# Optimization experiments

Measured on AMD Instinct MI355X. Metric: run time of the kernel, lower is better.

The kernel has to match this reference:

```python
import jax, jax.numpy as jnp
import numpy as np


def _w16_to_4():
    # Constant 4x16 projection from 16 gate logits to {1, A, B, A*B} coefficients
    W = np.zeros((4, 16), np.float32)
    W[0, 8:16] = 1
    W[1, [2, 3, 6, 7]] = 1
    W[1, [8, 9, 12, 13]] = -1
    W[2, [4, 5, 6, 7]] = 1
    W[2, [8, 9, 10, 11]] = -1
    W[3, 1] = 1
    W[3, 6] = -2
    W[3, [2, 4, 7, 14]] = -1
    W[3, [1, 8, 11, 13]] = 1
    W[3, 9] = 2
    return jnp.asarray(W)

W16_TO_4 = _w16_to_4()
G_SPARSITY = 1.0


def _layer(x, idx, w):
    # x: [B, in], idx: [2G] gather indices, w: [16, G]
    B = x.shape[0]
    xg = x[:, idx].reshape(B, -1, 2)          # [B, G, 2]
    A = xg[..., 0]
    Bv = xg[..., 1]
    s = jax.nn.softmax(w * G_SPARSITY, axis=0)  # [16, G]
    w4 = W16_TO_4 @ s                           # [4, G]
    return w4[0] + w4[1] * A + w4[2] * Bv + w4[3] * (A * Bv)  # [B, G]


def setup_inputs() -> dict:
    key = jax.random.key(0)
    B, IN, G, L = 2048, 1024, 16384, 6
    ks = jax.random.split(key, 2 * L + 3)
    inp = {"x": jax.random.uniform(ks[0], (B, IN), dtype=jnp.float32)}
    for l in range(L):
        hi = IN if l == 0 else G
        inp[f"idx{l}"] = jax.random.randint(ks[1 + l], (2 * G,), 0, hi, dtype=jnp.int32)
        inp[f"w{l}"] = jax.random.normal(ks[1 + L + l], (16, G), dtype=jnp.float32)
    inp["lin_w"] = jax.random.normal(ks[-2], (G, 1), dtype=jnp.float32) * 0.01
    inp["lin_b"] = jnp.zeros((1,), dtype=jnp.float32)
    return inp


def reference(x, w0, w1, w2, w3, w4, w5, lin_w, lin_b,
              idx0, idx1, idx2, idx3, idx4, idx5):
    ws = [w0, w1, w2, w3, w4, w5]
    idxs = [idx0, idx1, idx2, idx3, idx4, idx5]
    for w, idx in zip(ws, idxs):
        x = _layer(x, idx, w)
    return x @ lin_w + lin_b  # [B, 1]
```

## Files before the change

### kernel.cpp

```cpp
#include <hip/hip_runtime.h>
#include <hip/hip_fp16.h>

#define G_DIM 16384
#define N_BATCH 2048
#define IN_DIM 1024
#define NLAYER 6
#define THREADS 1024
#define GPT 16
#define CHUNK 4
#define NCHUNK (GPT / CHUNK)
#define ROWS 4

struct Ptrs {
    const int*   idx[NLAYER];
    const float* w[NLAYER];
};

__device__ __forceinline__ unsigned f2h(float a, float b) {
    __half2 h = __floats2half2_rn(a, b);
    return *reinterpret_cast<unsigned*>(&h);
}

__device__ __forceinline__ float mix_hlh(unsigned a, unsigned b, unsigned c) {
    float d;
    asm("v_fma_mix_f32 %0, %1, %2, %3 op_sel:[1,0,1] op_sel_hi:[1,1,1]"
        : "=v"(d) : "v"(a), "v"(b), "v"(c));
    return d;
}
__device__ __forceinline__ float mix_hhh(unsigned a, unsigned b, unsigned c) {
    float d;
    asm("v_fma_mix_f32 %0, %1, %2, %3 op_sel:[1,1,1] op_sel_hi:[1,1,1]"
        : "=v"(d) : "v"(a), "v"(b), "v"(c));
    return d;
}
__device__ __forceinline__ float mix_lll(unsigned a, unsigned b, unsigned c) {
    float d;
    asm("v_fma_mix_f32 %0, %1, %2, %3 op_sel:[0,0,0] op_sel_hi:[1,1,1]"
        : "=v"(d) : "v"(a), "v"(b), "v"(c));
    return d;
}
__device__ __forceinline__ float mix_lhl(unsigned a, unsigned b, unsigned c) {
    float d;
    asm("v_fma_mix_f32 %0, %1, %2, %3 op_sel:[0,1,0] op_sel_hi:[1,1,1]"
        : "=v"(d) : "v"(a), "v"(b), "v"(c));
    return d;
}
__device__ __forceinline__ float mix_alo(float u, unsigned A, float v) {
    float d;
    asm("v_fma_mix_f32 %0, %1, %2, %3 op_sel:[0,0,0] op_sel_hi:[0,1,0]"
        : "=v"(d) : "v"(u), "v"(A), "v"(v));
    return d;
}
__device__ __forceinline__ float mix_ahi(float u, unsigned A, float v) {
    float d;
    asm("v_fma_mix_f32 %0, %1, %2, %3 op_sel:[0,1,0] op_sel_hi:[0,1,0]"
        : "=v"(d) : "v"(u), "v"(A), "v"(v));
    return d;
}
__device__ __forceinline__ unsigned mix_pack(float u0, float v0, float u1, float v1,
                                             unsigned A) {
    unsigned t;
    asm("v_fma_mixlo_f16 %0, %1, %2, %3 op_sel:[0,0,0] op_sel_hi:[0,1,0]"
        : "=v"(t) : "v"(u0), "v"(A), "v"(v0));
    asm("v_fma_mixhi_f16 %0, %1, %2, %3 op_sel:[0,1,0] op_sel_hi:[0,1,0]"
        : "+v"(t) : "v"(u1), "v"(A), "v"(v1));
    return t;
}

__device__ __forceinline__ float4 softmax_coef(const float* __restrict__ w, int g) {
    float v[16];
    float m = -1e30f;
#pragma unroll
    for (int k = 0; k < 16; ++k) { v[k] = w[k * G_DIM + g]; m = fmaxf(m, v[k]); }
    float s = 0.f;
#pragma unroll
    for (int k = 0; k < 16; ++k) { v[k] = expf(v[k] - m); s += v[k]; }
    const float inv = 1.f / s;
    float4 c;
    c.x = (v[8]+v[9]+v[10]+v[11]+v[12]+v[13]+v[14]+v[15]) * inv;
    c.y = (v[2]+v[3]+v[6]+v[7] - v[8]-v[9]-v[12]-v[13]) * inv;
    c.z = (v[4]+v[5]+v[6]+v[7] - v[8]-v[9]-v[10]-v[11]) * inv;
    c.w = (v[1]-v[2]-v[4]-2.f*v[6]-v[7]+v[8]+2.f*v[9]+v[11]+v[13]-v[14]) * inv;
    return c;
}

__global__ __launch_bounds__(256) void pack_kernel(Ptrs P, uint2* __restrict__ hcf,
                                                   unsigned* __restrict__ sidx) {
    const int g = blockIdx.x * blockDim.x + threadIdx.x;
    const int l = blockIdx.y;
    const float4 c = softmax_coef(P.w[l], g);
    hcf[(size_t)l * G_DIM + g] = make_uint2(f2h(c.x, c.y), f2h(c.z, c.w));
    const int2 p = ((const int2*)P.idx[l])[g];
    sidx[(size_t)l * G_DIM + g] = (unsigned)p.x | ((unsigned)p.y << 16);
}

__global__ __launch_bounds__(THREADS) void fused_ws_kernel(
    const float* __restrict__ x,
    const uint2* __restrict__ hcf,
    const unsigned* __restrict__ sidx,
    const float* __restrict__ lin_w,
    const float* __restrict__ lin_b,
    float* __restrict__ out)
{
    __shared__ uint2 buf[G_DIM];
    __shared__ float red[ROWS][THREADS / 64];

    const int tid  = threadIdx.x;
    const int row0 = blockIdx.x * ROWS;

#pragma unroll
    for (int i = tid; i < IN_DIM; i += THREADS) {
        const float r0 = x[(size_t)(row0 + 0) * IN_DIM + i];
        const float r1 = x[(size_t)(row0 + 1) * IN_DIM + i];
        const float r2 = x[(size_t)(row0 + 2) * IN_DIM + i];
        const float r3 = x[(size_t)(row0 + 3) * IN_DIM + i];
        buf[i] = make_uint2(f2h(r0, r1), f2h(r2, r3));
    }

    unsigned pk[CHUNK];
    uint2    cc[CHUNK];
#pragma unroll
    for (int j = 0; j < CHUNK; ++j) {
        pk[j] = sidx[tid + j * THREADS];
        cc[j] = hcf[tid + j * THREADS];
    }

    __syncthreads();

    float a0 = 0.f, a1 = 0.f, a2 = 0.f, a3 = 0.f;

#pragma unroll
    for (int l = 0; l < NLAYER; ++l) {
        const uint2*    __restrict__ cl = hcf  + (size_t)l * G_DIM;
        const unsigned* __restrict__ sl = sidx + (size_t)l * G_DIM;
        uint2 o[GPT];

#pragma unroll
        for (int ch = 0; ch < NCHUNK; ++ch) {
            unsigned pkn[CHUNK];
            uint2    ccn[CHUNK];
            if (ch + 1 < NCHUNK) {
#pragma unroll
                for (int j = 0; j < CHUNK; ++j) {
                    pkn[j] = sl[tid + ((ch + 1) * CHUNK + j) * THREADS];
                    ccn[j] = cl[tid + ((ch + 1) * CHUNK + j) * THREADS];
                }
            } else if (l + 1 < NLAYER) {
                const unsigned* __restrict__ sn = sidx + (size_t)(l + 1) * G_DIM;
                const uint2*    __restrict__ cn = hcf  + (size_t)(l + 1) * G_DIM;
#pragma unroll
                for (int j = 0; j < CHUNK; ++j) {
                    pkn[j] = sn[tid + j * THREADS];
                    ccn[j] = cn[tid + j * THREADS];
                }
            }

            float lw[CHUNK];
            if (l == NLAYER - 1) {
#pragma unroll
                for (int j = 0; j < CHUNK; ++j)
                    lw[j] = lin_w[tid + (ch * CHUNK + j) * THREADS];
            }

#pragma unroll
            for (int j = 0; j < CHUNK; ++j) {
                const uint2 Au = buf[pk[j] & 0xFFFFu];
                const uint2 Bu = buf[pk[j] >> 16];
                const unsigned c01 = cc[j].x;
                const unsigned c23 = cc[j].y;
                const float u0 = mix_hlh(c23, Bu.x, c01);
                const float u1 = mix_hhh(c23, Bu.x, c01);
                const float v0 = mix_lll(c23, Bu.x, c01);
                const float v1 = mix_lhl(c23, Bu.x, c01);
                const float u2 = mix_hlh(c23, Bu.y, c01);
                const float u3 = mix_hhh(c23, Bu.y, c01);
                const float v2 = mix_lll(c23, Bu.y, c01);
                const float v3 = mix_lhl(c23, Bu.y, c01);
                if (l < NLAYER - 1) {
                    const unsigned t01 = mix_pack(u0, v0, u1, v1, Au.x);
                    const unsigned t23 = mix_pack(u2, v2, u3, v3, Au.y);
                    o[ch * CHUNK + j] = make_uint2(t01, t23);
                } else {
                    const float o0 = mix_alo(u0, Au.x, v0);
                    const float o1 = mix_ahi(u1, Au.x, v1);
                    const float o2 = mix_alo(u2, Au.y, v2);
                    const float o3 = mix_ahi(u3, Au.y, v3);
                    a0 = fmaf(o0, lw[j], a0);
                    a1 = fmaf(o1, lw[j], a1);
                    a2 = fmaf(o2, lw[j], a2);
                    a3 = fmaf(o3, lw[j], a3);
                }
            }

            if (ch + 1 < NCHUNK || l + 1 < NLAYER) {
#pragma unroll
                for (int j = 0; j < CHUNK; ++j) { pk[j] = pkn[j]; cc[j] = ccn[j]; }
            }
        }

        if (l < NLAYER - 1) {
            __syncthreads();
#pragma unroll
            for (int i = 0; i < GPT; ++i) buf[tid + i * THREADS] = o[i];
            __syncthreads();
        }
    }

#pragma unroll
    for (int off = 32; off > 0; off >>= 1) {
        a0 += __shfl_down(a0, off);
        a1 += __shfl_down(a1, off);
        a2 += __shfl_down(a2, off);
        a3 += __shfl_down(a3, off);
    }
    const int lane = tid & 63, wid = tid >> 6;
    if (lane == 0) { red[0][wid] = a0; red[1][wid] = a1; red[2][wid] = a2; red[3][wid] = a3; }
    __syncthreads();
    if (tid < ROWS) {
        float s = 0.f;
#pragma unroll
        for (int k = 0; k < THREADS / 64; ++k) s += red[tid][k];
        out[row0 + tid] = s + lin_b[0];
    }
}

__global__ __launch_bounds__(THREADS, 1) void fused_fallback_kernel(
    const float* __restrict__ x, Ptrs P,
    const float* __restrict__ lin_w, const float* __restrict__ lin_b,
    float* __restrict__ out)
{
    __shared__ float2 buf[G_DIM];
    __shared__ float red0[THREADS / 64];
    __shared__ float red1[THREADS / 64];
    const int tid  = threadIdx.x;
    const int row0 = blockIdx.x * 2;
    for (int i = tid; i < IN_DIM; i += THREADS)
        buf[i] = make_float2(x[(size_t)row0 * IN_DIM + i],
                             x[(size_t)(row0 + 1) * IN_DIM + i]);
    __syncthreads();
    float2 o[GPT];
    for (int l = 0; l < NLAYER; ++l) {
        const int2* __restrict__ idxl = (const int2*)P.idx[l];
#pragma unroll
        for (int i = 0; i < GPT; ++i) {
            const int g = tid + i * THREADS;
            const int2 p = idxl[g];
            const float4 c = softmax_coef(P.w[l], g);
            const float2 Ap = buf[p.x];
            const float2 Bp = buf[p.y];
            o[i].x = fmaf(fmaf(c.w, Bp.x, c.y), Ap.x, fmaf(c.z, Bp.x, c.x));
            o[i].y = fmaf(fmaf(c.w, Bp.y, c.y), Ap.y, fmaf(c.z, Bp.y, c.x));
        }
        __syncthreads();
#pragma unroll
        for (int i = 0; i < GPT; ++i) buf[tid + i * THREADS] = o[i];
        __syncthreads();
    }
    float a0 = 0.f, a1 = 0.f;
#pragma unroll
    for (int i = 0; i < GPT; ++i) {
        const int g = tid + i * THREADS;
        const float lw = lin_w[g];
        const float2 bv = buf[g];
        a0 = fmaf(bv.x, lw, a0);
        a1 = fmaf(bv.y, lw, a1);
    }
#pragma unroll
    for (int off = 32; off > 0; off >>= 1) {
        a0 += __shfl_down(a0, off);
        a1 += __shfl_down(a1, off);
    }
    const int lane = tid & 63, wid = tid >> 6;
    if (lane == 0) { red0[wid] = a0; red1[wid] = a1; }
    __syncthreads();
    if (tid == 0) {
        float s0 = 0.f, s1 = 0.f;
#pragma unroll
        for (int k = 0; k < THREADS / 64; ++k) { s0 += red0[k]; s1 += red1[k]; }
        const float lb = lin_b[0];
        out[row0]     = s0 + lb;
        out[row0 + 1] = s1 + lb;
    }
}

extern "C" void kernel_launch(void* const* d_in, const int* in_sizes, int n_in,
                              void* d_out, int out_size, void* d_ws, size_t ws_size,
                              hipStream_t stream) {
    const float* x = (const float*)d_in[0];
    Ptrs P;
    for (int l = 0; l < NLAYER; ++l) {
        P.idx[l] = (const int*)d_in[1 + 2 * l];
        P.w[l]   = (const float*)d_in[2 + 2 * l];
    }
    const float* lin_w = (const float*)d_in[13];
    const float* lin_b = (const float*)d_in[14];
    float* out = (float*)d_out;

    const size_t hcf_bytes  = (size_t)NLAYER * G_DIM * sizeof(uint2);
    const size_t sidx_bytes = (size_t)NLAYER * G_DIM * sizeof(unsigned);
    if (ws_size >= hcf_bytes + sidx_bytes) {
        uint2*    hcf  = (uint2*)d_ws;
        unsigned* sidx = (unsigned*)((char*)d_ws + hcf_bytes);
        dim3 cgrid(G_DIM / 256, NLAYER);
        pack_kernel<<<cgrid, 256, 0, stream>>>(P, hcf, sidx);
        fused_ws_kernel<<<N_BATCH / ROWS, THREADS, 0, stream>>>(
            x, hcf, sidx, lin_w, lin_b, out);
    } else {
        fused_fallback_kernel<<<N_BATCH / 2, THREADS, 0, stream>>>(
            x, P, lin_w, lin_b, out);
    }
}
```

Before: 56.36 us.

## Assign gate pairs per thread with vectorized loads and software-pipelined LDS gathers

Each thread now handles adjacent gate pairs, so index, coefficient, lin_w and LDS output traffic use 64/128-bit vector loads and stores (uint2/uint4/float2) instead of scalar ones. The gather from shared memory is software-pipelined: the next pair's A/B reads are issued before the current pair's FMA math. Global prefetch is staggered two chunks ahead for indices and one ahead for coefficients. The aim is fewer memory instructions and better latency hiding, at the cost of more live registers and a changed gate-to-thread mapping that can alter LDS bank conflict patterns.

```diff
diff --git a/kernel.cpp b/kernel.cpp
--- a/kernel.cpp
+++ b/kernel.cpp
@@ -6,9 +6,8 @@
 #define IN_DIM 1024
 #define NLAYER 6
 #define THREADS 1024
-#define GPT 16
-#define CHUNK 4
-#define NCHUNK (GPT / CHUNK)
+#define NPAIR 8
+#define NCHUNK 4
 #define ROWS 4
 
 struct Ptrs {
@@ -67,6 +66,45 @@
     return t;
 }
 
+struct PairG { uint2 A0, B0, A1, B1; };
+
+#define GATHER(G, PK)                                     \
+    do {                                                  \
+        (G).A0 = buf[(PK).x & 0xFFFFu];                   \
+        (G).B0 = buf[(PK).x >> 16];                       \
+        (G).A1 = buf[(PK).y & 0xFFFFu];                   \
+        (G).B1 = buf[(PK).y >> 16];                       \
+    } while (0)
+
+__device__ __forceinline__ uint2 gate_fma(uint2 Au, uint2 Bu, unsigned c01, unsigned c23) {
+    const float u0 = mix_hlh(c23, Bu.x, c01);
+    const float u1 = mix_hhh(c23, Bu.x, c01);
+    const float v0 = mix_lll(c23, Bu.x, c01);
+    const float v1 = mix_lhl(c23, Bu.x, c01);
+    const float u2 = mix_hlh(c23, Bu.y, c01);
+    const float u3 = mix_hhh(c23, Bu.y, c01);
+    const float v2 = mix_lll(c23, Bu.y, c01);
+    const float v3 = mix_lhl(c23, Bu.y, c01);
+    const unsigned t01 = mix_pack(u0, v0, u1, v1, Au.x);
+    const unsigned t23 = mix_pack(u2, v2, u3, v3, Au.y);
+    return make_uint2(t01, t23);
+}
+__device__ __forceinline__ void gate_acc(uint2 Au, uint2 Bu, unsigned c01, unsigned c23,
+                                         float lw, float& a0, float& a1, float& a2, float& a3) {
+    const float u0 = mix_hlh(c23, Bu.x, c01);
+    const float u1 = mix_hhh(c23, Bu.x, c01);
+    const float v0 = mix_lll(c23, Bu.x, c01);
+    const float v1 = mix_lhl(c23, Bu.x, c01);
+    const float u2 = mix_hlh(c23, Bu.y, c01);
+    const float u3 = mix_hhh(c23, Bu.y, c01);
+    const float v2 = mix_lll(c23, Bu.y, c01);
+    const float v3 = mix_lhl(c23, Bu.y, c01);
+    a0 = fmaf(mix_alo(u0, Au.x, v0), lw, a0);
+    a1 = fmaf(mix_ahi(u1, Au.x, v1), lw, a1);
+    a2 = fmaf(mix_alo(u2, Au.y, v2), lw, a2);
+    a3 = fmaf(mix_ahi(u3, Au.y, v3), lw, a3);
+}
+
 __device__ __forceinline__ float4 softmax_coef(const float* __restrict__ w, int g) {
     float v[16];
     float m = -1e30f;
@@ -102,13 +140,13 @@
     const float* __restrict__ lin_b,
     float* __restrict__ out)
 {
-    __shared__ uint2 buf[G_DIM];
+    __shared__ uint4 buf4[G_DIM / 2];
     __shared__ float red[ROWS][THREADS / 64];
+    uint2* buf = (uint2*)buf4;
 
     const int tid  = threadIdx.x;
     const int row0 = blockIdx.x * ROWS;
 
-#pragma unroll
     for (int i = tid; i < IN_DIM; i += THREADS) {
         const float r0 = x[(size_t)(row0 + 0) * IN_DIM + i];
         const float r1 = x[(size_t)(row0 + 1) * IN_DIM + i];
@@ -117,12 +155,17 @@
         buf[i] = make_uint2(f2h(r0, r1), f2h(r2, r3));
     }
 
-    unsigned pk[CHUNK];
-    uint2    cc[CHUNK];
-#pragma unroll
-    for (int j = 0; j < CHUNK; ++j) {
-        pk[j] = sidx[tid + j * THREADS];
-        cc[j] = hcf[tid + j * THREADS];
+    const uint2*  __restrict__ sidx2 = (const uint2*)sidx;
+    const uint4*  __restrict__ hcf4  = (const uint4*)hcf;
+    const float2* __restrict__ lw2   = (const float2*)lin_w;
+
+    uint2 pkA[2], pkB[2];
+    uint4 ccA[2];
+#pragma unroll
+    for (int j = 0; j < 2; ++j) {
+        pkA[j] = sidx2[tid + j * THREADS];
+        pkB[j] = sidx2[tid + (2 + j) * THREADS];
+        ccA[j] = hcf4 [tid + j * THREADS];
     }
 
     __syncthreads();
@@ -131,77 +174,67 @@
 
 #pragma unroll
     for (int l = 0; l < NLAYER; ++l) {
-        const uint2*    __restrict__ cl = hcf  + (size_t)l * G_DIM;
-        const unsigned* __restrict__ sl = sidx + (size_t)l * G_DIM;
-        uint2 o[GPT];
+        uint4 o[NPAIR];
+        PairG Gc, Gn;
+        GATHER(Gc, pkA[0]);
 
 #pragma unroll
         for (int ch = 0; ch < NCHUNK; ++ch) {
-            unsigned pkn[CHUNK];
-            uint2    ccn[CHUNK];
-            if (ch + 1 < NCHUNK) {
-#pragma unroll
-                for (int j = 0; j < CHUNK; ++j) {
-                    pkn[j] = sl[tid + ((ch + 1) * CHUNK + j) * THREADS];
-                    ccn[j] = cl[tid + ((ch + 1) * CHUNK + j) * THREADS];
-                }
-            } else if (l + 1 < NLAYER) {
-                const unsigned* __restrict__ sn = sidx + (size_t)(l + 1) * G_DIM;
-                const uint2*    __restrict__ cn = hcf  + (size_t)(l + 1) * G_DIM;
-#pragma unroll
-                for (int j = 0; j < CHUNK; ++j) {
-                    pkn[j] = sn[tid + j * THREADS];
-                    ccn[j] = cn[tid + j * THREADS];
-                }
-            }
-
-            float lw[CHUNK];
+            uint2 pkC[2];
+            uint4 ccB[2];
+            const bool haveC  = (ch + 2 < NCHUNK) || (l + 1 < NLAYER);
+            const bool haveB  = (ch + 1 < NCHUNK) || (l + 1 < NLAYER);
+            if (haveC) {
+                const int lc = (ch + 2 < NCHUNK) ? l : l + 1;
+                const int cc_ = (ch + 2 < NCHUNK) ? ch + 2 : ch + 2 - NCHUNK;
+                const uint2* sC = sidx2 + (size_t)lc * (G_DIM / 2);
+#pragma unroll
+                for (int j = 0; j < 2; ++j) pkC[j] = sC[tid + (cc_ * 2 + j) * THREADS];
+            }
+            if (haveB) {
+                const int lb = (ch + 1 < NCHUNK) ? l : l + 1;
+                const int cb = (ch + 1 < NCHUNK) ? ch + 1 : 0;
+                const uint4* cB = hcf4 + (size_t)lb * (G_DIM / 2);
+#pragma unroll
+                for (int j = 0; j < 2; ++j) ccB[j] = cB[tid + (cb * 2 + j) * THREADS];
+            }
+            float2 lwp[2];
             if (l == NLAYER - 1) {
 #pragma unroll
-                for (int j = 0; j < CHUNK; ++j)
-                    lw[j] = lin_w[tid + (ch * CHUNK + j) * THREADS];
-            }
-
-#pragma unroll
-            for (int j = 0; j < CHUNK; ++j) {
-                const uint2 Au = buf[pk[j] & 0xFFFFu];
-                const uint2 Bu = buf[pk[j] >> 16];
-                const unsigned c01 = cc[j].x;
-                const unsigned c23 = cc[j].y;
-                const float u0 = mix_hlh(c23, Bu.x, c01);
-                const float u1 = mix_hhh(c23, Bu.x, c01);
-                const float v0 = mix_lll(c23, Bu.x, c01);
-                const float v1 = mix_lhl(c23, Bu.x, c01);
-                const float u2 = mix_hlh(c23, Bu.y, c01);
-                const float u3 = mix_hhh(c23, Bu.y, c01);
-                const float v2 = mix_lll(c23, Bu.y, c01);
-                const float v3 = mix_lhl(c23, Bu.y, c01);
-                if (l < NLAYER - 1) {
-                    const unsigned t01 = mix_pack(u0, v0, u1, v1, Au.x);
-                    const unsigned t23 = mix_pack(u2, v2, u3, v3, Au.y);
-                    o[ch * CHUNK + j] = make_uint2(t01, t23);
-                } else {
-                    const float o0 = mix_alo(u0, Au.x, v0);
-                    const float o1 = mix_ahi(u1, Au.x, v1);
-                    const float o2 = mix_alo(u2, Au.y, v2);
-                    const float o3 = mix_ahi(u3, Au.y, v3);
-                    a0 = fmaf(o0, lw[j], a0);
-                    a1 = fmaf(o1, lw[j], a1);
-                    a2 = fmaf(o2, lw[j], a2);
-                    a3 = fmaf(o3, lw[j], a3);
-                }
-            }
-
-            if (ch + 1 < NCHUNK || l + 1 < NLAYER) {
-#pragma unroll
-                for (int j = 0; j < CHUNK; ++j) { pk[j] = pkn[j]; cc[j] = ccn[j]; }
+                for (int j = 0; j < 2; ++j) lwp[j] = lw2[tid + (ch * 2 + j) * THREADS];
+            }
+
+            GATHER(Gn, pkA[1]);
+            if (l < NLAYER - 1) {
+                const uint2 g0 = gate_fma(Gc.A0, Gc.B0, ccA[0].x, ccA[0].y);
+                const uint2 g1 = gate_fma(Gc.A1, Gc.B1, ccA[0].z, ccA[0].w);
+                o[ch * 2] = make_uint4(g0.x, g0.y, g1.x, g1.y);
+            } else {
+                gate_acc(Gc.A0, Gc.B0, ccA[0].x, ccA[0].y, lwp[0].x, a0, a1, a2, a3);
+                gate_acc(Gc.A1, Gc.B1, ccA[0].z, ccA[0].w, lwp[0].y, a0, a1, a2, a3);
+            }
+            if (ch + 1 < NCHUNK) GATHER(Gc, pkB[0]);
+            if (l < NLAYER - 1) {
+                const uint2 g0 = gate_fma(Gn.A0, Gn.B0, ccA[1].x, ccA[1].y);
+                const uint2 g1 = gate_fma(Gn.A1, Gn.B1, ccA[1].z, ccA[1].w);
+                o[ch * 2 + 1] = make_uint4(g0.x, g0.y, g1.x, g1.y);
+            } else {
+                gate_acc(Gn.A0, Gn.B0, ccA[1].x, ccA[1].y, lwp[1].x, a0, a1, a2, a3);
+                gate_acc(Gn.A1, Gn.B1, ccA[1].z, ccA[1].w, lwp[1].y, a0, a1, a2, a3);
+            }
+
+#pragma unroll
+            for (int j = 0; j < 2; ++j) {
+                pkA[j] = pkB[j];
+                if (haveC) pkB[j] = pkC[j];
+                if (haveB) ccA[j] = ccB[j];
             }
         }
 
         if (l < NLAYER - 1) {
             __syncthreads();
 #pragma unroll
-            for (int i = 0; i < GPT; ++i) buf[tid + i * THREADS] = o[i];
+            for (int p = 0; p < NPAIR; ++p) buf4[tid + p * THREADS] = o[p];
             __syncthreads();
         }
     }
@@ -238,11 +271,11 @@
         buf[i] = make_float2(x[(size_t)row0 * IN_DIM + i],
                              x[(size_t)(row0 + 1) * IN_DIM + i]);
     __syncthreads();
-    float2 o[GPT];
+    float2 o[16];
     for (int l = 0; l < NLAYER; ++l) {
         const int2* __restrict__ idxl = (const int2*)P.idx[l];
 #pragma unroll
-        for (int i = 0; i < GPT; ++i) {
+        for (int i = 0; i < 16; ++i) {
             const int g = tid + i * THREADS;
             const int2 p = idxl[g];
             const float4 c = softmax_coef(P.w[l], g);
@@ -253,12 +286,12 @@
         }
         __syncthreads();
 #pragma unroll
-        for (int i = 0; i < GPT; ++i) buf[tid + i * THREADS] = o[i];
+        for (int i = 0; i < 16; ++i) buf[tid + i * THREADS] = o[i];
         __syncthreads();
     }
     float a0 = 0.f, a1 = 0.f;
 #pragma unroll
-    for (int i = 0; i < GPT; ++i) {
+    for (int i = 0; i < 16; ++i) {
         const int g = tid + i * THREADS;
         const float lw = lin_w[g];
         const float2 bv = buf[g];
```

After: 52.91 us. 1.07x faster.
